# Kernel tuning notes

Hardware: AMD Instinct MI355X
Metric: run time of the kernel (lower is better)

The kernel has to match this reference:

```python
import jax, jax.numpy as jnp
import numpy as np

B, S, HID = 2, 2048, 768
H, DH = 12, 64
WINDOW = 128
THETA = 10000.0
NEG_INF = -1e9  # keras MHA uses -1e9 additive mask


def _rope(x, theta=THETA):
    """Apply rotary embedding. x: [B, S, H, DH] (rotate over last dim)."""
    s, d = x.shape[1], x.shape[-1]
    inv_freq = 1.0 / (theta ** (jnp.arange(0, d, 2, dtype=jnp.float32) / d))  # [d/2]
    ang = jnp.arange(s, dtype=jnp.float32)[:, None] * inv_freq[None, :]       # [S, d/2]
    cos = jnp.concatenate([jnp.cos(ang), jnp.cos(ang)], axis=-1)[None, :, None, :]  # [1,S,1,d]
    sin = jnp.concatenate([jnp.sin(ang), jnp.sin(ang)], axis=-1)[None, :, None, :]
    x1, x2 = x[..., : d // 2], x[..., d // 2 :]
    rot = jnp.concatenate([-x2, x1], axis=-1)
    return x * cos + rot * sin


def setup_inputs() -> dict:
    key = jax.random.key(0)
    ks = jax.random.split(key, 9)
    std = 0.02
    hidden_states = jax.random.normal(ks[0], (B, S, HID), dtype=jnp.float32)
    attention_mask = jnp.ones((B, S), dtype=jnp.int32)
    Wq = std * jax.random.truncated_normal(ks[1], -2.0, 2.0, (HID, H, DH), dtype=jnp.float32)
    Wk = std * jax.random.truncated_normal(ks[2], -2.0, 2.0, (HID, H, DH), dtype=jnp.float32)
    Wv = std * jax.random.truncated_normal(ks[3], -2.0, 2.0, (HID, H, DH), dtype=jnp.float32)
    Wo = std * jax.random.truncated_normal(ks[4], -2.0, 2.0, (H, DH, HID), dtype=jnp.float32)
    bq = jnp.zeros((H, DH), dtype=jnp.float32)
    bk = jnp.zeros((H, DH), dtype=jnp.float32)
    bv = jnp.zeros((H, DH), dtype=jnp.float32)
    bo = jnp.zeros((HID,), dtype=jnp.float32)
    return {"hidden_states": hidden_states, "attention_mask": attention_mask,
            "Wq": Wq, "bq": bq, "Wk": Wk, "bk": bk, "Wv": Wv, "bv": bv, "Wo": Wo, "bo": bo}


def reference(hidden_states, attention_mask, Wq, bq, Wk, bk, Wv, bv, Wo, bo):
    b, s, _ = hidden_states.shape
    # RoPE applied to raw hidden states split into heads (as in source), then flattened back
    x4 = hidden_states.reshape(b, s, H, DH)
    q_in = _rope(x4).reshape(b, s, HID)
    k_in = _rope(x4).reshape(b, s, HID)
    v_in = hidden_states
    # keras MultiHeadAttention projections
    q = jnp.einsum("bsi,ihd->bshd", q_in, Wq) + bq
    k = jnp.einsum("bsi,ihd->bshd", k_in, Wk) + bk
    v = jnp.einsum("bsi,ihd->bshd", v_in, Wv) + bv
    q = q * (1.0 / jnp.sqrt(jnp.float32(DH)))
    scores = jnp.einsum("bqhd,bkhd->bhqk", q, k)  # [B,H,S,S]
    # combined mask: padding [B,1,1,S] AND sliding window [S,S]
    pad = attention_mask.astype(bool)[:, None, None, :]
    pos = jnp.arange(s, dtype=jnp.int32)
    win = (jnp.abs(pos[:, None] - pos[None, :]) < WINDOW)[None, None, :, :]
    mask = jnp.logical_and(pad, win)
    scores = scores + (1.0 - mask.astype(scores.dtype)) * NEG_INF
    attn = jax.nn.softmax(scores, axis=-1)
    out = jnp.einsum("bhqk,bkhd->bqhd", attn, v)
    return jnp.einsum("bqhd,hdi->bqi", out, Wo) + bo
```

## Files before the change

kernel.cpp:

```cpp
#include <hip/hip_runtime.h>
#include <hip/hip_bf16.h>
#include <math.h>

#define NB 2
#define NS 2048
#define NHID 768
#define NH 12
#define NDH 64
#define NWIN 128

typedef __attribute__((ext_vector_type(8))) short bf16x8;
typedef __attribute__((ext_vector_type(4))) float f32x4;

__device__ inline unsigned short f2b(float f) {
    union { float f; unsigned int i; } x; x.f = f;
    unsigned int r = x.i + 0x7FFFu + ((x.i >> 16) & 1u);
    return (unsigned short)(r >> 16);
}
__device__ inline int xcd_remap(int flat, int nwg) {
    return (flat & 7) * (nwg >> 3) + (flat >> 3);
}
__device__ __forceinline__ void gload_lds16(const void* g, void* l) {
    __builtin_amdgcn_global_load_lds((const __attribute__((address_space(1))) void*)g,
                                     (__attribute__((address_space(3))) void*)l, 16, 0, 0);
}

union Frag { bf16x8 v; unsigned long long q[2]; uint4 u; };

__global__ __launch_bounds__(256) void k_prep(const float* __restrict__ x,
                                              __hip_bfloat16* __restrict__ rb,
                                              __hip_bfloat16* __restrict__ xb,
                                              const float* __restrict__ w0, const float* __restrict__ w1,
                                              const float* __restrict__ w2, const float* __restrict__ w3,
                                              __hip_bfloat16* o0, __hip_bfloat16* o1,
                                              __hip_bfloat16* o2, __hip_bfloat16* o3) {
    int bid = blockIdx.x;
    int t = threadIdx.x;
    if (bid < 576) {
        int wsel = bid / 144, r = bid % 144;
        int kx = r % 12, ny = r / 12;
        const float* W; __hip_bfloat16* O;
        switch (wsel) {
            case 0: W = w0; O = o0; break;
            case 1: W = w1; O = o1; break;
            case 2: W = w2; O = o2; break;
            default: W = w3; O = o3; break;
        }
        __shared__ float tile[64][65];
        int k0 = kx * 64, n0 = ny * 64;
        int rr = t >> 4, cc = (t & 15) * 4;
#pragma unroll
        for (int u = 0; u < 4; ++u) {
            int row = rr + u * 16;
            float4 f = *(const float4*)(W + (size_t)(k0 + row) * NHID + n0 + cc);
            tile[row][cc] = f.x; tile[row][cc + 1] = f.y;
            tile[row][cc + 2] = f.z; tile[row][cc + 3] = f.w;
        }
        __syncthreads();
#pragma unroll
        for (int u = 0; u < 4; ++u) {
            int n = rr + u * 16;
            ushort4 s = { f2b(tile[cc + 0][n]), f2b(tile[cc + 1][n]),
                          f2b(tile[cc + 2][n]), f2b(tile[cc + 3][n]) };
            *(ushort4*)((unsigned short*)O + (size_t)(n0 + n) * NHID + k0 + cc) = s;
        }
    } else {
        int idx = (bid - 576) * 256 + t;
        int f = idx & 31;
        int h = (idx >> 5) % NH;
        int bs = idx / (32 * NH);
        int s = bs & (NS - 1);
        int base = bs * NHID + h * NDH;
        float x1 = x[base + f], x2 = x[base + 32 + f];
        float inv = exp2f(-0.4152410118609203f * (float)f);
        float ang = (float)s * inv;
        float c = cosf(ang), sn = sinf(ang);
        ((unsigned short*)rb)[base + f]      = f2b(x1 * c - x2 * sn);
        ((unsigned short*)rb)[base + 32 + f] = f2b(x2 * c + x1 * sn);
        ((unsigned short*)xb)[base + f]      = f2b(x1);
        ((unsigned short*)xb)[base + 32 + f] = f2b(x2);
    }
}

__device__ __forceinline__ void gemm128(const __hip_bfloat16* __restrict__ A,
                                        const __hip_bfloat16* __restrict__ Wt,
                                        const float* __restrict__ bias,
                                        __hip_bfloat16* __restrict__ Cb,
                                        float scale, int m0, int n0) {
    __shared__ __attribute__((aligned(16))) unsigned short As[128][64];
    __shared__ __attribute__((aligned(16))) unsigned short Bs[128][64];
    const int t = threadIdx.x;
    const int wid = t >> 6, lane = t & 63;
    const int wm = (wid >> 1) * 64, wn = (wid & 1) * 64;
    const int g = lane >> 4, r16 = lane & 15;
    const int swz = r16 & 7;

    f32x4 acc[4][4];
#pragma unroll
    for (int i = 0; i < 4; ++i)
#pragma unroll
        for (int j = 0; j < 4; ++j) acc[i][j] = (f32x4){0.f, 0.f, 0.f, 0.f};

    const int srow = t >> 3;
    const int gslot = (t & 7) ^ (srow & 7);
    const unsigned short* gA = (const unsigned short*)A + (size_t)(m0 + srow) * NHID + gslot * 8;
    const unsigned short* gB = (const unsigned short*)Wt + (size_t)(n0 + srow) * NHID + gslot * 8;
    char* lA = (char*)&As[0][0] + wid * 1024;
    char* lB = (char*)&Bs[0][0] + wid * 1024;

    for (int ks = 0; ks < NHID / 64; ++ks) {
        __syncthreads();
#pragma unroll
        for (int c = 0; c < 4; ++c)
            gload_lds16(gA + (size_t)c * 32 * NHID + ks * 64, lA + c * 4096);
#pragma unroll
        for (int c = 0; c < 4; ++c)
            gload_lds16(gB + (size_t)c * 32 * NHID + ks * 64, lB + c * 4096);
        __syncthreads();
#pragma unroll
        for (int kk = 0; kk < 2; ++kk) {
            Frag af[4], bf[4];
#pragma unroll
            for (int mi = 0; mi < 4; ++mi)
                af[mi].u = *(const uint4*)&As[wm + mi * 16 + r16][((kk * 4 + g) ^ swz) * 8];
#pragma unroll
            for (int ni = 0; ni < 4; ++ni)
                bf[ni].u = *(const uint4*)&Bs[wn + ni * 16 + r16][((kk * 4 + g) ^ swz) * 8];
#pragma unroll
            for (int mi = 0; mi < 4; ++mi)
#pragma unroll
                for (int ni = 0; ni < 4; ++ni)
                    acc[mi][ni] = __builtin_amdgcn_mfma_f32_16x16x32_bf16(af[mi].v, bf[ni].v, acc[mi][ni], 0, 0, 0);
        }
    }

#pragma unroll
    for (int mi = 0; mi < 4; ++mi)
#pragma unroll
        for (int ni = 0; ni < 4; ++ni)
#pragma unroll
            for (int r = 0; r < 4; ++r) {
                int m = m0 + wm + mi * 16 + 4 * g + r;
                int n = n0 + wn + ni * 16 + r16;
                float v = (acc[mi][ni][r] + bias[n]) * scale;
                ((unsigned short*)Cb)[(size_t)m * NHID + n] = f2b(v);
            }
}

__global__ __launch_bounds__(256) void k_gemm_qkv(const __hip_bfloat16* __restrict__ rb,
                                                  const __hip_bfloat16* __restrict__ xb,
                                                  const __hip_bfloat16* __restrict__ WtQ,
                                                  const __hip_bfloat16* __restrict__ WtK,
                                                  const __hip_bfloat16* __restrict__ WtV,
                                                  const float* __restrict__ bq,
                                                  const float* __restrict__ bk,
                                                  const float* __restrict__ bv,
                                                  __hip_bfloat16* qb, __hip_bfloat16* kb,
                                                  __hip_bfloat16* vb) {
    int flat = blockIdx.x + 6 * blockIdx.y + 192 * blockIdx.z;
    int id = xcd_remap(flat, 576);
    int z = id / 192, rem = id - z * 192;
    int ty = rem / 6, tx = rem - ty * 6;
    const __hip_bfloat16 *A, *W; const float* bias; __hip_bfloat16* C; float scale;
    switch (z) {
        case 0:  A = rb; W = WtQ; bias = bq; C = qb; scale = 0.125f; break;
        case 1:  A = rb; W = WtK; bias = bk; C = kb; scale = 1.0f;   break;
        default: A = xb; W = WtV; bias = bv; C = vb; scale = 1.0f;   break;
    }
    gemm128(A, W, bias, C, scale, ty * 128, tx * 128);
}

template<int MF>
__device__ __forceinline__ void gemm_body(const __hip_bfloat16* __restrict__ A,
                                          const __hip_bfloat16* __restrict__ Wt,
                                          const float* __restrict__ bias,
                                          __hip_bfloat16* __restrict__ Cb,
                                          float* __restrict__ Cf, float scale,
                                          int m0, int n0) {
    constexpr int BM = 32 * MF;
    __shared__ __attribute__((aligned(16))) unsigned short As[BM][64];
    __shared__ __attribute__((aligned(16))) unsigned short Bs[64][64];
    const int t = threadIdx.x;
    const int wid = t >> 6, lane = t & 63;
    const int wm = (wid >> 1) * 16 * MF, wn = (wid & 1) * 32;
    const int g = lane >> 4, r16 = lane & 15;
    const int swz = r16 & 7;

    f32x4 acc[MF][2];
#pragma unroll
    for (int i = 0; i < MF; ++i)
#pragma unroll
        for (int j = 0; j < 2; ++j) acc[i][j] = (f32x4){0.f, 0.f, 0.f, 0.f};

    const int srow = t >> 3;
    const int gslot = (t & 7) ^ (srow & 7);
    const unsigned short* gA = (const unsigned short*)A + (size_t)(m0 + srow) * NHID + gslot * 8;
    const unsigned short* gB = (const unsigned short*)Wt + (size_t)(n0 + srow) * NHID + gslot * 8;
    char* lA = (char*)&As[0][0] + wid * 1024;
    char* lB = (char*)&Bs[0][0] + wid * 1024;

    for (int ks = 0; ks < NHID / 64; ++ks) {
        __syncthreads();
#pragma unroll
        for (int c = 0; c < MF; ++c)
            gload_lds16(gA + (size_t)c * 32 * NHID + ks * 64, lA + c * 4096);
#pragma unroll
        for (int c = 0; c < 2; ++c)
            gload_lds16(gB + (size_t)c * 32 * NHID + ks * 64, lB + c * 4096);
        __syncthreads();
#pragma unroll
        for (int kk = 0; kk < 2; ++kk) {
            Frag af[MF], bf[2];
#pragma unroll
            for (int mi = 0; mi < MF; ++mi)
                af[mi].u = *(const uint4*)&As[wm + mi * 16 + r16][((kk * 4 + g) ^ swz) * 8];
#pragma unroll
            for (int ni = 0; ni < 2; ++ni)
                bf[ni].u = *(const uint4*)&Bs[wn + ni * 16 + r16][((kk * 4 + g) ^ swz) * 8];
#pragma unroll
            for (int mi = 0; mi < MF; ++mi)
#pragma unroll
                for (int ni = 0; ni < 2; ++ni)
                    acc[mi][ni] = __builtin_amdgcn_mfma_f32_16x16x32_bf16(af[mi].v, bf[ni].v, acc[mi][ni], 0, 0, 0);
        }
    }

#pragma unroll
    for (int mi = 0; mi < MF; ++mi)
#pragma unroll
        for (int ni = 0; ni < 2; ++ni)
#pragma unroll
            for (int r = 0; r < 4; ++r) {
                int m = m0 + wm + mi * 16 + 4 * g + r;
                int n = n0 + wn + ni * 16 + r16;
                float v = (acc[mi][ni][r] + bias[n]) * scale;
                if (Cb) ((unsigned short*)Cb)[(size_t)m * NHID + n] = f2b(v);
                else    Cf[(size_t)m * NHID + n] = v;
            }
}

__global__ __launch_bounds__(256) void k_gemm_out(const __hip_bfloat16* __restrict__ A,
                                                  const __hip_bfloat16* __restrict__ Wt,
                                                  const float* __restrict__ bias,
                                                  float* __restrict__ Cf) {
    int flat = blockIdx.x + 12 * blockIdx.y;
    int id = xcd_remap(flat, 768);
    int ty = id / 12, tx = id - ty * 12;
    gemm_body<2>(A, Wt, bias, nullptr, Cf, 1.0f, ty * 64, tx * 64);
}

__global__ __launch_bounds__(256) void k_attn(const __hip_bfloat16* __restrict__ q,
                                              const __hip_bfloat16* __restrict__ kmat,
                                              const __hip_bfloat16* __restrict__ vmat,
                                              const int* __restrict__ am,
                                              __hip_bfloat16* __restrict__ o) {
    __shared__ unsigned short Ks[2][64][72];
    __shared__ unsigned short Vt[2][64][72];
    __shared__ float kmask[2][64];
    const int t = threadIdx.x;
    const int h = blockIdx.y, b = blockIdx.z;
    const int i0 = blockIdx.x * 64;
    const int w = t >> 6, lane = t & 63;
    const int g = lane >> 4, r16 = lane & 15;
    const int qrow = i0 + w * 16 + r16;

    Frag qf[2];
    {
        const unsigned short* qp = (const unsigned short*)q + ((size_t)(b * NS) + qrow) * NHID + h * NDH;
        qf[0].q[0] = *(const unsigned long long*)(qp + 4 * g);
        qf[0].q[1] = *(const unsigned long long*)(qp + 16 + 4 * g);
        qf[1].q[0] = *(const unsigned long long*)(qp + 32 + 4 * g);
        qf[1].q[1] = *(const unsigned long long*)(qp + 48 + 4 * g);
    }
    float m_run = -1e30f, l_run = 0.f;
    f32x4 oacc[4];
#pragma unroll
    for (int i = 0; i < 4; ++i) oacc[i] = (f32x4){0.f, 0.f, 0.f, 0.f};

    const int ktL = (i0 == 0) ? 2 : (i0 == 64) ? 1 : 0;
    const int ktH = (i0 == NS - 64) ? 2 : (i0 == NS - 128) ? 3 : 4;

    uint4 pK0, pK1, pV0, pV1; float pm = 0.f;

#define LOADREGS(KT) do {                                                        \
    int j0_ = i0 - 128 + (KT) * 64;                                              \
    const unsigned short* kp_ = (const unsigned short*)kmat +                    \
        ((size_t)(b * NS) + j0_ + (t >> 2)) * NHID + h * NDH + (t & 3) * 16;     \
    pK0 = *(const uint4*)kp_;                                                    \
    pK1 = *(const uint4*)(kp_ + 8);                                              \
    const unsigned short* vp_ = (const unsigned short*)vmat +                    \
        ((size_t)(b * NS) + j0_ + 2 * (t & 31)) * NHID + h * NDH + (t >> 5) * 8; \
    pV0 = *(const uint4*)vp_;                                                    \
    pV1 = *(const uint4*)(vp_ + NHID);                                           \
    if (t < 64) pm = (am[b * NS + j0_ + t] != 0) ? 0.f : -1e30f;                 \
} while (0)

    LOADREGS(ktL);
    for (int kt = ktL; kt <= ktH; ++kt) {
        const int j0 = i0 - 128 + kt * 64;
        const int b2 = kt & 1;
        {
            *(uint4*)&Ks[b2][t >> 2][(t & 3) * 16]     = pK0;
            *(uint4*)&Ks[b2][t >> 2][(t & 3) * 16 + 8] = pK1;
            union { uint4 u; unsigned short s[8]; } a0, a1;
            a0.u = pV0; a1.u = pV1;
#pragma unroll
            for (int e = 0; e < 8; ++e) {
                unsigned int pk = (unsigned int)a0.s[e] | ((unsigned int)a1.s[e] << 16);
                *(unsigned int*)&Vt[b2][(t >> 5) * 8 + e][2 * (t & 31)] = pk;
            }
            if (t < 64) kmask[b2][t] = pm;
        }
        if (kt < ktH) LOADREGS(kt + 1);
        asm volatile("s_waitcnt lgkmcnt(0)" ::: "memory");
        __builtin_amdgcn_s_barrier();

        f32x4 sacc[4];
#pragma unroll
        for (int i = 0; i < 4; ++i) sacc[i] = (f32x4){0.f, 0.f, 0.f, 0.f};
#pragma unroll
        for (int mi = 0; mi < 4; ++mi) {
            Frag kf0, kf1;
            const unsigned short* pk = &Ks[b2][mi * 16 + r16][0];
            kf0.q[0] = *(const unsigned long long*)(pk + 4 * g);
            kf0.q[1] = *(const unsigned long long*)(pk + 16 + 4 * g);
            kf1.q[0] = *(const unsigned long long*)(pk + 32 + 4 * g);
            kf1.q[1] = *(const unsigned long long*)(pk + 48 + 4 * g);
            sacc[mi] = __builtin_amdgcn_mfma_f32_16x16x32_bf16(kf0.v, qf[0].v, sacc[mi], 0, 0, 0);
            sacc[mi] = __builtin_amdgcn_mfma_f32_16x16x32_bf16(kf1.v, qf[1].v, sacc[mi], 0, 0, 0);
        }

        float p[4][4];
        float tmax = -1e30f;
#pragma unroll
        for (int mi = 0; mi < 4; ++mi)
#pragma unroll
            for (int r = 0; r < 4; ++r) {
                int key = j0 + mi * 16 + 4 * g + r;
                float s = sacc[mi][r] + kmask[b2][mi * 16 + 4 * g + r];
                int d = qrow - key; d = d < 0 ? -d : d;
                if (d >= NWIN) s = -1e30f;
                p[mi][r] = s;
                tmax = fmaxf(tmax, s);
            }
        tmax = fmaxf(tmax, __shfl_xor(tmax, 16));
        tmax = fmaxf(tmax, __shfl_xor(tmax, 32));
        float mnew = fmaxf(m_run, tmax);
        float psum = 0.f;
#pragma unroll
        for (int mi = 0; mi < 4; ++mi)
#pragma unroll
            for (int r = 0; r < 4; ++r) {
                float pv = __expf(p[mi][r] - mnew);
                p[mi][r] = pv;
                psum += pv;
            }
        psum += __shfl_xor(psum, 16);
        psum += __shfl_xor(psum, 32);
        float alpha = __expf(m_run - mnew);
        m_run = mnew;
        l_run = l_run * alpha + psum;
#pragma unroll
        for (int mi = 0; mi < 4; ++mi)
#pragma unroll
            for (int r = 0; r < 4; ++r) oacc[mi][r] *= alpha;

        Frag pf[2];
#pragma unroll
        for (int ks2 = 0; ks2 < 2; ++ks2) {
            union { bf16x8 v; unsigned short s[8]; } pp;
#pragma unroll
            for (int r = 0; r < 4; ++r) {
                pp.s[r]     = f2b(p[2 * ks2][r]);
                pp.s[r + 4] = f2b(p[2 * ks2 + 1][r]);
            }
            pf[ks2].v = pp.v;
        }

#pragma unroll
        for (int mi = 0; mi < 4; ++mi) {
            Frag vf0, vf1;
            const unsigned short* pv = &Vt[b2][mi * 16 + r16][0];
            vf0.q[0] = *(const unsigned long long*)(pv + 4 * g);
            vf0.q[1] = *(const unsigned long long*)(pv + 16 + 4 * g);
            vf1.q[0] = *(const unsigned long long*)(pv + 32 + 4 * g);
            vf1.q[1] = *(const unsigned long long*)(pv + 48 + 4 * g);
            oacc[mi] = __builtin_amdgcn_mfma_f32_16x16x32_bf16(vf0.v, pf[0].v, oacc[mi], 0, 0, 0);
            oacc[mi] = __builtin_amdgcn_mfma_f32_16x16x32_bf16(vf1.v, pf[1].v, oacc[mi], 0, 0, 0);
        }
    }
#undef LOADREGS

    float inv_l = 1.0f / l_run;
    unsigned short* op = (unsigned short*)o + ((size_t)(b * NS) + qrow) * NHID + h * NDH;
#pragma unroll
    for (int mi = 0; mi < 4; ++mi) {
        ushort4 s = { f2b(oacc[mi][0] * inv_l), f2b(oacc[mi][1] * inv_l),
                      f2b(oacc[mi][2] * inv_l), f2b(oacc[mi][3] * inv_l) };
        *(ushort4*)(op + mi * 16 + 4 * g) = s;
    }
}

extern "C" void kernel_launch(void* const* d_in, const int* in_sizes, int n_in,
                              void* d_out, int out_size, void* d_ws, size_t ws_size,
                              hipStream_t stream) {
    (void)in_sizes; (void)n_in; (void)out_size; (void)ws_size;
    const float* x  = (const float*)d_in[0];
    const int*   am = (const int*)d_in[1];
    const float* Wq = (const float*)d_in[2];
    const float* bq = (const float*)d_in[3];
    const float* Wk = (const float*)d_in[4];
    const float* bk = (const float*)d_in[5];
    const float* Wv = (const float*)d_in[6];
    const float* bv = (const float*)d_in[7];
    const float* Wo = (const float*)d_in[8];
    const float* bo = (const float*)d_in[9];
    float* out = (float*)d_out;
    float* ws  = (float*)d_ws;

    __hip_bfloat16* rb  = (__hip_bfloat16*)(ws);
    __hip_bfloat16* xb  = (__hip_bfloat16*)(ws + 1572864);
    __hip_bfloat16* WtQ = (__hip_bfloat16*)(ws + 3145728);
    __hip_bfloat16* WtK = (__hip_bfloat16*)(ws + 3440640);
    __hip_bfloat16* WtV = (__hip_bfloat16*)(ws + 3735552);
    __hip_bfloat16* WtO = (__hip_bfloat16*)(ws + 4030464);
    __hip_bfloat16* qb  = (__hip_bfloat16*)(ws + 4325376);
    __hip_bfloat16* kb  = (__hip_bfloat16*)(ws + 5898240);
    __hip_bfloat16* vb  = (__hip_bfloat16*)(ws + 7471104);
    __hip_bfloat16* aob = (__hip_bfloat16*)(ws + 9043968);

    k_prep<<<576 + 6144, 256, 0, stream>>>(x, rb, xb, Wq, Wk, Wv, Wo, WtQ, WtK, WtV, WtO);
    dim3 gq(6, 32, 3);
    k_gemm_qkv<<<gq, 256, 0, stream>>>(rb, xb, WtQ, WtK, WtV, bq, bk, bv, qb, kb, vb);
    dim3 ga(NS / 64, NH, NB);
    k_attn<<<ga, 256, 0, stream>>>(qb, kb, vb, am, aob);
    dim3 gg(NHID / 64, NB * NS / 64);
    k_gemm_out<<<gg, 256, 0, stream>>>(aob, WtO, bo, out);
}
```

Before: 64.02 us.

## Fuse Q and K projections sharing the RoPE input tile in QKV GEMM

Replaces the three separate 128x128 GEMM tiles for Q, K and V with a fused Q+K body that loads each 128-row tile of the rotated input once and multiplies it against both WtQ and WtK (64 columns each). V is computed by a separate 128x64 gemm_body<4> path. The launch grid changes from 576 blocks of 128x128 to 768 blocks of 128x64, intended to cut redundant A-tile loads and improve occupancy balance. The tiles per block are smaller, which lowers per-block compute intensity on the V path.

```diff
diff --git a/kernel.cpp b/kernel.cpp
--- a/kernel.cpp
+++ b/kernel.cpp
@@ -82,94 +82,6 @@
     }
 }
 
-__device__ __forceinline__ void gemm128(const __hip_bfloat16* __restrict__ A,
-                                        const __hip_bfloat16* __restrict__ Wt,
-                                        const float* __restrict__ bias,
-                                        __hip_bfloat16* __restrict__ Cb,
-                                        float scale, int m0, int n0) {
-    __shared__ __attribute__((aligned(16))) unsigned short As[128][64];
-    __shared__ __attribute__((aligned(16))) unsigned short Bs[128][64];
-    const int t = threadIdx.x;
-    const int wid = t >> 6, lane = t & 63;
-    const int wm = (wid >> 1) * 64, wn = (wid & 1) * 64;
-    const int g = lane >> 4, r16 = lane & 15;
-    const int swz = r16 & 7;
-
-    f32x4 acc[4][4];
-#pragma unroll
-    for (int i = 0; i < 4; ++i)
-#pragma unroll
-        for (int j = 0; j < 4; ++j) acc[i][j] = (f32x4){0.f, 0.f, 0.f, 0.f};
-
-    const int srow = t >> 3;
-    const int gslot = (t & 7) ^ (srow & 7);
-    const unsigned short* gA = (const unsigned short*)A + (size_t)(m0 + srow) * NHID + gslot * 8;
-    const unsigned short* gB = (const unsigned short*)Wt + (size_t)(n0 + srow) * NHID + gslot * 8;
-    char* lA = (char*)&As[0][0] + wid * 1024;
-    char* lB = (char*)&Bs[0][0] + wid * 1024;
-
-    for (int ks = 0; ks < NHID / 64; ++ks) {
-        __syncthreads();
-#pragma unroll
-        for (int c = 0; c < 4; ++c)
-            gload_lds16(gA + (size_t)c * 32 * NHID + ks * 64, lA + c * 4096);
-#pragma unroll
-        for (int c = 0; c < 4; ++c)
-            gload_lds16(gB + (size_t)c * 32 * NHID + ks * 64, lB + c * 4096);
-        __syncthreads();
-#pragma unroll
-        for (int kk = 0; kk < 2; ++kk) {
-            Frag af[4], bf[4];
-#pragma unroll
-            for (int mi = 0; mi < 4; ++mi)
-                af[mi].u = *(const uint4*)&As[wm + mi * 16 + r16][((kk * 4 + g) ^ swz) * 8];
-#pragma unroll
-            for (int ni = 0; ni < 4; ++ni)
-                bf[ni].u = *(const uint4*)&Bs[wn + ni * 16 + r16][((kk * 4 + g) ^ swz) * 8];
-#pragma unroll
-            for (int mi = 0; mi < 4; ++mi)
-#pragma unroll
-                for (int ni = 0; ni < 4; ++ni)
-                    acc[mi][ni] = __builtin_amdgcn_mfma_f32_16x16x32_bf16(af[mi].v, bf[ni].v, acc[mi][ni], 0, 0, 0);
-        }
-    }
-
-#pragma unroll
-    for (int mi = 0; mi < 4; ++mi)
-#pragma unroll
-        for (int ni = 0; ni < 4; ++ni)
-#pragma unroll
-            for (int r = 0; r < 4; ++r) {
-                int m = m0 + wm + mi * 16 + 4 * g + r;
-                int n = n0 + wn + ni * 16 + r16;
-                float v = (acc[mi][ni][r] + bias[n]) * scale;
-                ((unsigned short*)Cb)[(size_t)m * NHID + n] = f2b(v);
-            }
-}
-
-__global__ __launch_bounds__(256) void k_gemm_qkv(const __hip_bfloat16* __restrict__ rb,
-                                                  const __hip_bfloat16* __restrict__ xb,
-                                                  const __hip_bfloat16* __restrict__ WtQ,
-                                                  const __hip_bfloat16* __restrict__ WtK,
-                                                  const __hip_bfloat16* __restrict__ WtV,
-                                                  const float* __restrict__ bq,
-                                                  const float* __restrict__ bk,
-                                                  const float* __restrict__ bv,
-                                                  __hip_bfloat16* qb, __hip_bfloat16* kb,
-                                                  __hip_bfloat16* vb) {
-    int flat = blockIdx.x + 6 * blockIdx.y + 192 * blockIdx.z;
-    int id = xcd_remap(flat, 576);
-    int z = id / 192, rem = id - z * 192;
-    int ty = rem / 6, tx = rem - ty * 6;
-    const __hip_bfloat16 *A, *W; const float* bias; __hip_bfloat16* C; float scale;
-    switch (z) {
-        case 0:  A = rb; W = WtQ; bias = bq; C = qb; scale = 0.125f; break;
-        case 1:  A = rb; W = WtK; bias = bk; C = kb; scale = 1.0f;   break;
-        default: A = xb; W = WtV; bias = bv; C = vb; scale = 1.0f;   break;
-    }
-    gemm128(A, W, bias, C, scale, ty * 128, tx * 128);
-}
-
 template<int MF>
 __device__ __forceinline__ void gemm_body(const __hip_bfloat16* __restrict__ A,
                                           const __hip_bfloat16* __restrict__ Wt,
@@ -237,6 +149,105 @@
                 if (Cb) ((unsigned short*)Cb)[(size_t)m * NHID + n] = f2b(v);
                 else    Cf[(size_t)m * NHID + n] = v;
             }
+}
+
+__device__ __forceinline__ void qk_body(const __hip_bfloat16* __restrict__ A,
+                                        const __hip_bfloat16* __restrict__ WtQ,
+                                        const __hip_bfloat16* __restrict__ WtK,
+                                        const float* __restrict__ bq,
+                                        const float* __restrict__ bk,
+                                        __hip_bfloat16* __restrict__ Cq,
+                                        __hip_bfloat16* __restrict__ Ck,
+                                        int m0, int n0) {
+    __shared__ __attribute__((aligned(16))) unsigned short As[128][64];
+    __shared__ __attribute__((aligned(16))) unsigned short BsQ[64][64];
+    __shared__ __attribute__((aligned(16))) unsigned short BsK[64][64];
+    const int t = threadIdx.x;
+    const int wid = t >> 6, lane = t & 63;
+    const int wm = (wid >> 1) * 64, wn = (wid & 1) * 32;
+    const int g = lane >> 4, r16 = lane & 15;
+    const int swz = r16 & 7;
+
+    f32x4 aq[4][2], ak[4][2];
+#pragma unroll
+    for (int i = 0; i < 4; ++i)
+#pragma unroll
+        for (int j = 0; j < 2; ++j) {
+            aq[i][j] = (f32x4){0.f, 0.f, 0.f, 0.f};
+            ak[i][j] = (f32x4){0.f, 0.f, 0.f, 0.f};
+        }
+
+    const int srow = t >> 3;
+    const int gslot = (t & 7) ^ (srow & 7);
+    const unsigned short* gA  = (const unsigned short*)A   + (size_t)(m0 + srow) * NHID + gslot * 8;
+    const unsigned short* gBQ = (const unsigned short*)WtQ + (size_t)(n0 + srow) * NHID + gslot * 8;
+    const unsigned short* gBK = (const unsigned short*)WtK + (size_t)(n0 + srow) * NHID + gslot * 8;
+    char* lA  = (char*)&As[0][0]  + wid * 1024;
+    char* lBQ = (char*)&BsQ[0][0] + wid * 1024;
+    char* lBK = (char*)&BsK[0][0] + wid * 1024;
+
+    for (int ks = 0; ks < NHID / 64; ++ks) {
+        __syncthreads();
+#pragma unroll
+        for (int c = 0; c < 4; ++c)
+            gload_lds16(gA + (size_t)c * 32 * NHID + ks * 64, lA + c * 4096);
+#pragma unroll
+        for (int c = 0; c < 2; ++c)
+            gload_lds16(gBQ + (size_t)c * 32 * NHID + ks * 64, lBQ + c * 4096);
+#pragma unroll
+        for (int c = 0; c < 2; ++c)
+            gload_lds16(gBK + (size_t)c * 32 * NHID + ks * 64, lBK + c * 4096);
+        __syncthreads();
+#pragma unroll
+        for (int kk = 0; kk < 2; ++kk) {
+            Frag af[4], bq_[2], bk_[2];
+#pragma unroll
+            for (int mi = 0; mi < 4; ++mi)
+                af[mi].u = *(const uint4*)&As[wm + mi * 16 + r16][((kk * 4 + g) ^ swz) * 8];
+#pragma unroll
+            for (int ni = 0; ni < 2; ++ni) {
+                bq_[ni].u = *(const uint4*)&BsQ[wn + ni * 16 + r16][((kk * 4 + g) ^ swz) * 8];
+                bk_[ni].u = *(const uint4*)&BsK[wn + ni * 16 + r16][((kk * 4 + g) ^ swz) * 8];
+            }
+#pragma unroll
+            for (int mi = 0; mi < 4; ++mi)
+#pragma unroll
+                for (int ni = 0; ni < 2; ++ni) {
+                    aq[mi][ni] = __builtin_amdgcn_mfma_f32_16x16x32_bf16(af[mi].v, bq_[ni].v, aq[mi][ni], 0, 0, 0);
+                    ak[mi][ni] = __builtin_amdgcn_mfma_f32_16x16x32_bf16(af[mi].v, bk_[ni].v, ak[mi][ni], 0, 0, 0);
+                }
+        }
+    }
+
+#pragma unroll
+    for (int mi = 0; mi < 4; ++mi)
+#pragma unroll
+        for (int ni = 0; ni < 2; ++ni)
+#pragma unroll
+            for (int r = 0; r < 4; ++r) {
+                int m = m0 + wm + mi * 16 + 4 * g + r;
+                int n = n0 + wn + ni * 16 + r16;
+                ((unsigned short*)Cq)[(size_t)m * NHID + n] = f2b((aq[mi][ni][r] + bq[n]) * 0.125f);
+                ((unsigned short*)Ck)[(size_t)m * NHID + n] = f2b(ak[mi][ni][r] + bk[n]);
+            }
+}
+
+__global__ __launch_bounds__(256) void k_gemm_qkv(const __hip_bfloat16* __restrict__ rb,
+                                                  const __hip_bfloat16* __restrict__ xb,
+                                                  const __hip_bfloat16* __restrict__ WtQ,
+                                                  const __hip_bfloat16* __restrict__ WtK,
+                                                  const __hip_bfloat16* __restrict__ WtV,
+                                                  const float* __restrict__ bq,
+                                                  const float* __restrict__ bk,
+                                                  const float* __restrict__ bv,
+                                                  __hip_bfloat16* qb, __hip_bfloat16* kb,
+                                                  __hip_bfloat16* vb) {
+    int id = xcd_remap(blockIdx.x, 384);
+    int ty = id / 12, tx = id % 12;
+    if (blockIdx.y == 0)
+        qk_body(rb, WtQ, WtK, bq, bk, qb, kb, ty * 128, tx * 64);
+    else
+        gemm_body<4>(xb, WtV, bv, vb, nullptr, 1.0f, ty * 128, tx * 64);
 }
 
 __global__ __launch_bounds__(256) void k_gemm_out(const __hip_bfloat16* __restrict__ A,
@@ -430,7 +441,7 @@
     __hip_bfloat16* aob = (__hip_bfloat16*)(ws + 9043968);
 
     k_prep<<<576 + 6144, 256, 0, stream>>>(x, rb, xb, Wq, Wk, Wv, Wo, WtQ, WtK, WtV, WtO);
-    dim3 gq(6, 32, 3);
+    dim3 gq(384, 2);
     k_gemm_qkv<<<gq, 256, 0, stream>>>(rb, xb, WtQ, WtK, WtV, bq, bk, bv, qb, kb, vb);
     dim3 ga(NS / 64, NH, NB);
     k_attn<<<ga, 256, 0, stream>>>(qb, kb, vb, am, aob);
```

Result: slower. 70.60 us (+10.3%).
